# Kernel optimization log

Measured on AMD Instinct MI355X. Metric: run time of the kernel, lower is better.

## Reference

```python
import jax, jax.numpy as jnp
import numpy as np
import math

BS = 8  # JPEG block size
QUALITY = 250.0  # __scale_quality(20) = 5000/20
OFFSET = 128.0 / 255.0


def _dctmtx(bs=BS):
    m = np.empty((bs, bs), dtype=np.float32)
    for j in range(bs):
        for i in range(bs):
            if i == 0:
                m[i, j] = 1.0 / math.sqrt(bs)
            else:
                m[i, j] = math.sqrt(2.0 / bs) * math.cos(math.pi * (2 * j + 1) * i / (2 * bs))
    return jnp.asarray(m)


XFORM = jnp.array([[0.299, 0.587, 0.114],
                   [-0.168735892, -0.331264108, 0.5],
                   [0.5, -0.418687589, -0.081312411]], dtype=jnp.float32)


def setup_inputs() -> dict:
    key = jax.random.key(0)
    k1, k2 = jax.random.split(key)
    rgb = jax.random.uniform(k1, (16, 3, 512, 512), dtype=jnp.float32)
    # qtable: round(abs(t)+0.5)/255 -> positive integers / 255
    quantize = jax.random.randint(k2, (3, BS, BS), 1, 100).astype(jnp.float32) / 255.0
    return {"rgb": rgb, "quantize": quantize}


def _blockify(x, bs=BS):
    # x: [B, H, W] -> [B, H//bs, W//bs, bs, bs]
    b, h, w = x.shape
    return x.reshape(b, h // bs, bs, w // bs, bs).transpose(0, 1, 3, 2, 4)


def reference(rgb, quantize):
    B, C, H, W = rgb.shape
    dct = _dctmtx()
    # RGB -> YCbCr (BHWC matmul with xform^T, expressed on BCHW via einsum)
    ycbcr = jnp.einsum('bchw,kc->bkhw', rgb, XFORM)
    shift = jnp.array([0.0, OFFSET, OFFSET], dtype=rgb.dtype)[None, :, None, None]
    ycbcr = jnp.clip(ycbcr + shift, 0.0, 1.0) - OFFSET
    # chroma 2x2 mean subsample
    y = ycbcr[:, 0]                                            # [B, H, W]
    cbcr = ycbcr[:, 1:].reshape(B, 2, H // 2, 2, W // 2, 2).mean(axis=(3, 5))
    channels = [y, cbcr[:, 0], cbcr[:, 1]]
    outs = []
    for i, ch in enumerate(channels):
        blocks = _blockify(ch)                                 # [B, nh, nw, 8, 8]
        dcts = jnp.einsum('ij,bhwjk,lk->bhwil', dct, blocks, dct)
        denom = quantize[i] * (QUALITY / 100.0) + 0.5 / 255.0  # [8, 8]
        comp = jnp.round(dcts / denom)
        outs.append(comp.reshape(-1, BS, BS))
    return tuple(outs)
```

## Files before the change

kernel.cpp:

```cpp
#include <hip/hip_runtime.h>
#include <math.h>


static __device__ __forceinline__ float clip01(float v) {
    return fminf(fmaxf(v, 0.0f), 1.0f);
}

#define M1f 0.49039264020161522f
#define M2f 0.46193976625564337f
#define M3f 0.41573480615127262f
#define M4f 0.35355339059327376f
#define M5f 0.27778511650980111f
#define M6f 0.19134171618254489f
#define M7f 0.097545161008064134f

static constexpr float Dm[8][8] = {
    { M4f,  M4f,  M4f,  M4f,  M4f,  M4f,  M4f,  M4f},
    { M1f,  M3f,  M5f,  M7f, -M7f, -M5f, -M3f, -M1f},
    { M2f,  M6f, -M6f, -M2f, -M2f, -M6f,  M6f,  M2f},
    { M3f, -M7f, -M1f, -M5f,  M5f,  M1f,  M7f, -M3f},
    { M4f, -M4f, -M4f,  M4f,  M4f, -M4f, -M4f,  M4f},
    { M5f, -M1f,  M7f,  M3f, -M3f, -M7f,  M1f, -M5f},
    { M6f, -M2f,  M2f, -M6f, -M6f,  M2f, -M2f,  M6f},
    { M7f, -M5f,  M3f, -M1f,  M1f, -M3f,  M5f, -M7f},
};

__global__ __launch_bounds__(256)
void jpeg_kernel(const float* __restrict__ rgb, const float* __restrict__ quant,
                 float* __restrict__ out)
{
    __shared__ __align__(16) float smem[3616];
    constexpr int YTT = 0;
    constexpr int CBT = 1152;
    constexpr int CRT = 1472;
    constexpr int QNT = 1792;
    constexpr int TMP = 1984;

    const int t = threadIdx.x;

    if (t < 192) smem[QNT + t] = quant[t];

    const int wg   = blockIdx.x;
    const int b    = wg >> 8;
    const int tile = wg & 255;
    const int th   = tile >> 4;
    const int tw   = tile & 15;

    {
        const int qr = t >> 4;
        const int qc = t & 15;
        const int r0 = 2 * qr, c0 = 2 * qc;
        const float* p = rgb + ((size_t)b * 3) * 262144 + (size_t)(th * 32 + r0) * 512 + (tw * 32 + c0);
        const float2 R0 = *(const float2*)p;
        const float2 R1 = *(const float2*)(p + 512);
        const float2 G0 = *(const float2*)(p + 262144);
        const float2 G1 = *(const float2*)(p + 262144 + 512);
        const float2 B0 = *(const float2*)(p + 524288);
        const float2 B1 = *(const float2*)(p + 524288 + 512);
        const float OFF = (float)(128.0 / 255.0);
        const float rr[4] = {R0.x, R0.y, R1.x, R1.y};
        const float gg[4] = {G0.x, G0.y, G1.x, G1.y};
        const float bb[4] = {B0.x, B0.y, B1.x, B1.y};
        float yv[4], cbv[4], crv[4];
        #pragma unroll
        for (int k = 0; k < 4; ++k) {
            const float r_ = rr[k], g_ = gg[k], b_ = bb[k];
            const float y  = (float)(0.299) * r_ + (float)(0.587) * g_ + (float)(0.114) * b_;
            const float cb = (float)(-0.168735892) * r_ + (float)(-0.331264108) * g_ + 0.5f * b_;
            const float cr = 0.5f * r_ + (float)(-0.418687589) * g_ + (float)(-0.081312411) * b_;
            yv[k]  = clip01(y) - OFF;
            cbv[k] = clip01(cb + OFF);
            crv[k] = clip01(cr + OFF);
        }
        *(float2*)&smem[YTT + c0 * 36 + r0]       = make_float2(yv[0], yv[2]);
        *(float2*)&smem[YTT + (c0 + 1) * 36 + r0] = make_float2(yv[1], yv[3]);
        float sb = cbv[0];
        sb = sb + cbv[1];
        sb = sb + cbv[2];
        sb = sb + cbv[3];
        smem[CBT + qc * 20 + qr] = sb * 0.25f - OFF;
        float sr = crv[0];
        sr = sr + crv[1];
        sr = sr + crv[2];
        sr = sr + crv[3];
        smem[CRT + qc * 20 + qr] = sr * 0.25f - OFF;
    }
    __syncthreads();

    const int w  = t >> 6;
    const int l  = t & 63;
    const int bi = l >> 3;
    const int lc = l & 7;

    if (bi < 6) {
        const int sb = w * 6 + bi;
        int xaddr, ch; size_t obase;
        if (sb < 16) {
            const int sr = sb >> 2, sc = sb & 3;
            xaddr = YTT + (sc * 8 + lc) * 36 + sr * 8; ch = 0;
            obase = (((size_t)(b * 64 + th * 4 + sr)) * 64 + (tw * 4 + sc)) * 64;
        } else if (sb < 20) {
            const int s = sb - 16, sr = s >> 1, sc = s & 1;
            xaddr = CBT + (sc * 8 + lc) * 20 + sr * 8; ch = 1;
            obase = (size_t)4194304 + (((size_t)(b * 32 + th * 2 + sr)) * 32 + (tw * 2 + sc)) * 64;
        } else {
            const int s = sb - 20, sr = s >> 1, sc = s & 1;
            xaddr = CRT + (sc * 8 + lc) * 20 + sr * 8; ch = 2;
            obase = (size_t)5242880 + (((size_t)(b * 32 + th * 2 + sr)) * 32 + (tw * 2 + sc)) * 64;
        }

        float x[8];
        *(float4*)&x[0] = *(const float4*)&smem[xaddr];
        *(float4*)&x[4] = *(const float4*)&smem[xaddr + 4];
        const int tbase = TMP + w * 408 + bi * 68;
        #pragma unroll
        for (int i = 0; i < 8; ++i) {
            float s = 0.0f;
            #pragma unroll
            for (int j = 0; j < 8; ++j) s += Dm[i][j] * x[j];
            smem[tbase + i * 8 + lc] = s;
        }

        float tr[8], q[8];
        *(float4*)&tr[0] = *(const float4*)&smem[tbase + lc * 8];
        *(float4*)&tr[4] = *(const float4*)&smem[tbase + lc * 8 + 4];
        *(float4*)&q[0]  = *(const float4*)&smem[QNT + ch * 64 + lc * 8];
        *(float4*)&q[4]  = *(const float4*)&smem[QNT + ch * 64 + lc * 8 + 4];

        const float qadd = (float)(0.5 / 255.0);
        float o[8];
        #pragma unroll
        for (int cc = 0; cc < 8; ++cc) {
            float s = 0.0f;
            #pragma unroll
            for (int k = 0; k < 8; ++k) s += tr[k] * Dm[cc][k];
            const float den = __fadd_rn(__fmul_rn(q[cc], 2.5f), qadd);
            o[cc] = rintf(s / den);
        }
        float* op = out + obase + lc * 8;
        *(float4*)&op[0] = make_float4(o[0], o[1], o[2], o[3]);
        *(float4*)&op[4] = make_float4(o[4], o[5], o[6], o[7]);
    }
}

extern "C" void kernel_launch(void* const* d_in, const int* in_sizes, int n_in,
                              void* d_out, int out_size, void* d_ws, size_t ws_size,
                              hipStream_t stream) {
    const float* rgb   = (const float*)d_in[0];
    const float* quant = (const float*)d_in[1];
    float* out = (float*)d_out;
    dim3 grid(4096), block(256);
    hipLaunchKernelGGL(jpeg_kernel, grid, block, 0, stream, rgb, quant, out);
}
```

Measured before the change: 17.97 us.

## Split tiles into single-wavefront 16x16 workgroups and drop block barrier

Each 32x32 tile is now handled by four separate 64-thread workgroups, each owning one 16x16 region: four Y blocks plus one Cb and one Cr block. Because the workgroup is a single wavefront, the __syncthreads between the color conversion and the DCT is removed and shared memory shrinks from 3616 to 920 floats. The quantization table is read straight from global memory into registers instead of being staged in LDS, and the global loads are issued earlier so they overlap the address setup. The cost is four times as many workgroups with 25% of lanes idle in the DCT stage, and correctness now depends on implicit wavefront-synchronous ordering of the LDS accesses.

```diff
diff --git a/kernel.cpp b/kernel.cpp
--- a/kernel.cpp
+++ b/kernel.cpp
@@ -25,38 +25,63 @@
     { M7f, -M5f,  M3f, -M1f,  M1f, -M3f,  M5f, -M7f},
 };
 
-__global__ __launch_bounds__(256)
+__global__ __launch_bounds__(64)
 void jpeg_kernel(const float* __restrict__ rgb, const float* __restrict__ quant,
                  float* __restrict__ out)
 {
-    __shared__ __align__(16) float smem[3616];
+    __shared__ __align__(16) float smem[920];
     constexpr int YTT = 0;
-    constexpr int CBT = 1152;
-    constexpr int CRT = 1472;
-    constexpr int QNT = 1792;
-    constexpr int TMP = 1984;
+    constexpr int CBT = 320;
+    constexpr int CRT = 416;
+    constexpr int TMP = 512;
 
-    const int t = threadIdx.x;
+    const int l  = threadIdx.x;
+    const int wg = blockIdx.x;
+    const int w  = wg & 3;
+    const int tw = (wg >> 2) & 15;
+    const int th = (wg >> 6) & 15;
+    const int b  = wg >> 10;
+    const int wr = w >> 1, wc = w & 1;
 
-    if (t < 192) smem[QNT + t] = quant[t];
+    const int qr = l >> 3;
+    const int qc = l & 7;
+    const int bi = l >> 3;
+    const int lc = l & 7;
 
-    const int wg   = blockIdx.x;
-    const int b    = wg >> 8;
-    const int tile = wg & 255;
-    const int th   = tile >> 4;
-    const int tw   = tile & 15;
+    const int prow = th * 32 + wr * 16 + 2 * qr;
+    const int pcol = tw * 32 + wc * 16 + 2 * qc;
+    const float* p = rgb + (size_t)b * 786432 + (size_t)prow * 512 + pcol;
+    const float2 R0 = *(const float2*)p;
+    const float2 R1 = *(const float2*)(p + 512);
+    const float2 G0 = *(const float2*)(p + 262144);
+    const float2 G1 = *(const float2*)(p + 262656);
+    const float2 B0 = *(const float2*)(p + 524288);
+    const float2 B1 = *(const float2*)(p + 524800);
+
+    float q[8];
+    int xaddr = 0; size_t obase = 0;
+    if (bi < 6) {
+        int ch;
+        if (bi < 4) {
+            const int bsr = bi >> 1, bsc = bi & 1;
+            xaddr = YTT + (bsc * 8 + lc) * 20 + bsr * 8; ch = 0;
+            obase = (((size_t)(b * 64 + th * 4 + wr * 2 + bsr)) * 64
+                     + (tw * 4 + wc * 2 + bsc)) * 64;
+        } else if (bi == 4) {
+            xaddr = CBT + lc * 12; ch = 1;
+            obase = (size_t)4194304
+                  + (((size_t)(b * 32 + th * 2 + wr)) * 32 + (tw * 2 + wc)) * 64;
+        } else {
+            xaddr = CRT + lc * 12; ch = 2;
+            obase = (size_t)5242880
+                  + (((size_t)(b * 32 + th * 2 + wr)) * 32 + (tw * 2 + wc)) * 64;
+        }
+        const float* qp = quant + ch * 64 + lc * 8;
+        *(float4*)&q[0] = *(const float4*)qp;
+        *(float4*)&q[4] = *(const float4*)(qp + 4);
+    }
 
     {
-        const int qr = t >> 4;
-        const int qc = t & 15;
-        const int r0 = 2 * qr, c0 = 2 * qc;
-        const float* p = rgb + ((size_t)b * 3) * 262144 + (size_t)(th * 32 + r0) * 512 + (tw * 32 + c0);
-        const float2 R0 = *(const float2*)p;
-        const float2 R1 = *(const float2*)(p + 512);
-        const float2 G0 = *(const float2*)(p + 262144);
-        const float2 G1 = *(const float2*)(p + 262144 + 512);
-        const float2 B0 = *(const float2*)(p + 524288);
-        const float2 B1 = *(const float2*)(p + 524288 + 512);
         const float OFF = (float)(128.0 / 255.0);
         const float rr[4] = {R0.x, R0.y, R1.x, R1.y};
         const float gg[4] = {G0.x, G0.y, G1.x, G1.y};
@@ -72,47 +97,25 @@
             cbv[k] = clip01(cb + OFF);
             crv[k] = clip01(cr + OFF);
         }
-        *(float2*)&smem[YTT + c0 * 36 + r0]       = make_float2(yv[0], yv[2]);
-        *(float2*)&smem[YTT + (c0 + 1) * 36 + r0] = make_float2(yv[1], yv[3]);
+        *(float2*)&smem[YTT + (2 * qc) * 20 + 2 * qr]     = make_float2(yv[0], yv[2]);
+        *(float2*)&smem[YTT + (2 * qc + 1) * 20 + 2 * qr] = make_float2(yv[1], yv[3]);
         float sb = cbv[0];
         sb = sb + cbv[1];
         sb = sb + cbv[2];
         sb = sb + cbv[3];
-        smem[CBT + qc * 20 + qr] = sb * 0.25f - OFF;
+        smem[CBT + qc * 12 + qr] = sb * 0.25f - OFF;
         float sr = crv[0];
         sr = sr + crv[1];
         sr = sr + crv[2];
         sr = sr + crv[3];
-        smem[CRT + qc * 20 + qr] = sr * 0.25f - OFF;
+        smem[CRT + qc * 12 + qr] = sr * 0.25f - OFF;
     }
-    __syncthreads();
-
-    const int w  = t >> 6;
-    const int l  = t & 63;
-    const int bi = l >> 3;
-    const int lc = l & 7;
 
     if (bi < 6) {
-        const int sb = w * 6 + bi;
-        int xaddr, ch; size_t obase;
-        if (sb < 16) {
-            const int sr = sb >> 2, sc = sb & 3;
-            xaddr = YTT + (sc * 8 + lc) * 36 + sr * 8; ch = 0;
-            obase = (((size_t)(b * 64 + th * 4 + sr)) * 64 + (tw * 4 + sc)) * 64;
-        } else if (sb < 20) {
-            const int s = sb - 16, sr = s >> 1, sc = s & 1;
-            xaddr = CBT + (sc * 8 + lc) * 20 + sr * 8; ch = 1;
-            obase = (size_t)4194304 + (((size_t)(b * 32 + th * 2 + sr)) * 32 + (tw * 2 + sc)) * 64;
-        } else {
-            const int s = sb - 20, sr = s >> 1, sc = s & 1;
-            xaddr = CRT + (sc * 8 + lc) * 20 + sr * 8; ch = 2;
-            obase = (size_t)5242880 + (((size_t)(b * 32 + th * 2 + sr)) * 32 + (tw * 2 + sc)) * 64;
-        }
-
         float x[8];
         *(float4*)&x[0] = *(const float4*)&smem[xaddr];
         *(float4*)&x[4] = *(const float4*)&smem[xaddr + 4];
-        const int tbase = TMP + w * 408 + bi * 68;
+        const int tbase = TMP + bi * 68;
         #pragma unroll
         for (int i = 0; i < 8; ++i) {
             float s = 0.0f;
@@ -121,11 +124,9 @@
             smem[tbase + i * 8 + lc] = s;
         }
 
-        float tr[8], q[8];
+        float tr[8];
         *(float4*)&tr[0] = *(const float4*)&smem[tbase + lc * 8];
         *(float4*)&tr[4] = *(const float4*)&smem[tbase + lc * 8 + 4];
-        *(float4*)&q[0]  = *(const float4*)&smem[QNT + ch * 64 + lc * 8];
-        *(float4*)&q[4]  = *(const float4*)&smem[QNT + ch * 64 + lc * 8 + 4];
 
         const float qadd = (float)(0.5 / 255.0);
         float o[8];
@@ -149,6 +150,6 @@
     const float* rgb   = (const float*)d_in[0];
     const float* quant = (const float*)d_in[1];
     float* out = (float*)d_out;
-    dim3 grid(4096), block(256);
+    dim3 grid(16384), block(64);
     hipLaunchKernelGGL(jpeg_kernel, grid, block, 0, stream, rgb, quant, out);
 }
```

Measured after the change: 25.68 us. 42.9% more time.

## Process two tiles per block and prefetch second tile during first DCT

Applied to the files above, without the earlier changes.

Each workgroup now handles two adjacent 32x32 tiles using double-buffered shared memory. The second tile's RGB loads are issued before the first tile's DCT, so global memory latency overlaps with compute. The quantization denominators are computed once and reused for both tiles, and the grid is halved. In exchange, the kernel holds more registers and shared memory per block, which may lower occupancy.

```diff
diff --git a/kernel.cpp b/kernel.cpp
--- a/kernel.cpp
+++ b/kernel.cpp
@@ -25,122 +25,155 @@
     { M7f, -M5f,  M3f, -M1f,  M1f, -M3f,  M5f, -M7f},
 };
 
+struct RGB6 { float2 R0, R1, G0, G1, B0, B1; };
+
+static __device__ __forceinline__ RGB6 load_quad(const float* __restrict__ rgb,
+                                                 int b, int prow, int pcol) {
+    const float* p = rgb + (size_t)b * 786432 + (size_t)prow * 512 + pcol;
+    RGB6 v;
+    v.R0 = *(const float2*)p;
+    v.R1 = *(const float2*)(p + 512);
+    v.G0 = *(const float2*)(p + 262144);
+    v.G1 = *(const float2*)(p + 262656);
+    v.B0 = *(const float2*)(p + 524288);
+    v.B1 = *(const float2*)(p + 524800);
+    return v;
+}
+
+static __device__ __forceinline__ void color_store(const RGB6& v, float* smem,
+    int ybase, int cbbase, int crbase, int qr, int qc)
+{
+    const float OFF = (float)(128.0 / 255.0);
+    const float rr[4] = {v.R0.x, v.R0.y, v.R1.x, v.R1.y};
+    const float gg[4] = {v.G0.x, v.G0.y, v.G1.x, v.G1.y};
+    const float bb[4] = {v.B0.x, v.B0.y, v.B1.x, v.B1.y};
+    float yv[4], cbv[4], crv[4];
+    #pragma unroll
+    for (int k = 0; k < 4; ++k) {
+        const float r_ = rr[k], g_ = gg[k], b_ = bb[k];
+        const float y  = (float)(0.299) * r_ + (float)(0.587) * g_ + (float)(0.114) * b_;
+        const float cb = (float)(-0.168735892) * r_ + (float)(-0.331264108) * g_ + 0.5f * b_;
+        const float cr = 0.5f * r_ + (float)(-0.418687589) * g_ + (float)(-0.081312411) * b_;
+        yv[k]  = clip01(y) - OFF;
+        cbv[k] = clip01(cb + OFF);
+        crv[k] = clip01(cr + OFF);
+    }
+    const int r0 = 2 * qr, c0 = 2 * qc;
+    *(float2*)&smem[ybase + c0 * 36 + r0]       = make_float2(yv[0], yv[2]);
+    *(float2*)&smem[ybase + (c0 + 1) * 36 + r0] = make_float2(yv[1], yv[3]);
+    float sb = cbv[0];
+    sb = sb + cbv[1];
+    sb = sb + cbv[2];
+    sb = sb + cbv[3];
+    smem[cbbase + qc * 20 + qr] = sb * 0.25f - OFF;
+    float sr = crv[0];
+    sr = sr + crv[1];
+    sr = sr + crv[2];
+    sr = sr + crv[3];
+    smem[crbase + qc * 20 + qr] = sr * 0.25f - OFF;
+}
+
+static __device__ __forceinline__ void dct_tile(float* smem, float* __restrict__ out,
+    int ybase, int cbbase, int crbase, int tmpbase, const float* den,
+    int b, int th, int tw, int sb, int lc)
+{
+    int xaddr; size_t obase;
+    if (sb < 16) {
+        const int sr = sb >> 2, sc = sb & 3;
+        xaddr = ybase + (sc * 8 + lc) * 36 + sr * 8;
+        obase = (((size_t)(b * 64 + th * 4 + sr)) * 64 + (tw * 4 + sc)) * 64;
+    } else if (sb < 20) {
+        const int s = sb - 16, sr = s >> 1, sc = s & 1;
+        xaddr = cbbase + (sc * 8 + lc) * 20 + sr * 8;
+        obase = (size_t)4194304 + (((size_t)(b * 32 + th * 2 + sr)) * 32 + (tw * 2 + sc)) * 64;
+    } else {
+        const int s = sb - 20, sr = s >> 1, sc = s & 1;
+        xaddr = crbase + (sc * 8 + lc) * 20 + sr * 8;
+        obase = (size_t)5242880 + (((size_t)(b * 32 + th * 2 + sr)) * 32 + (tw * 2 + sc)) * 64;
+    }
+    float x[8];
+    *(float4*)&x[0] = *(const float4*)&smem[xaddr];
+    *(float4*)&x[4] = *(const float4*)&smem[xaddr + 4];
+    #pragma unroll
+    for (int i = 0; i < 8; ++i) {
+        float s = 0.0f;
+        #pragma unroll
+        for (int j = 0; j < 8; ++j) s += Dm[i][j] * x[j];
+        smem[tmpbase + i * 8 + lc] = s;
+    }
+    float tr[8];
+    *(float4*)&tr[0] = *(const float4*)&smem[tmpbase + lc * 8];
+    *(float4*)&tr[4] = *(const float4*)&smem[tmpbase + lc * 8 + 4];
+    float o[8];
+    #pragma unroll
+    for (int cc = 0; cc < 8; ++cc) {
+        float s = 0.0f;
+        #pragma unroll
+        for (int k = 0; k < 8; ++k) s += tr[k] * Dm[cc][k];
+        o[cc] = rintf(s / den[cc]);
+    }
+    float* op = out + obase + lc * 8;
+    *(float4*)&op[0] = make_float4(o[0], o[1], o[2], o[3]);
+    *(float4*)&op[4] = make_float4(o[4], o[5], o[6], o[7]);
+}
+
 __global__ __launch_bounds__(256)
 void jpeg_kernel(const float* __restrict__ rgb, const float* __restrict__ quant,
                  float* __restrict__ out)
 {
-    __shared__ __align__(16) float smem[3616];
-    constexpr int YTT = 0;
-    constexpr int CBT = 1152;
-    constexpr int CRT = 1472;
-    constexpr int QNT = 1792;
-    constexpr int TMP = 1984;
+    __shared__ __align__(16) float smem[5408];
+    constexpr int YTT0 = 0;
+    constexpr int YTT1 = 1152;
+    constexpr int CBT0 = 2304;
+    constexpr int CBT1 = 2624;
+    constexpr int CRT0 = 2944;
+    constexpr int CRT1 = 3264;
+    constexpr int QNT  = 3584;
+    constexpr int TMP  = 3776;
 
     const int t = threadIdx.x;
 
     if (t < 192) smem[QNT + t] = quant[t];
 
-    const int wg   = blockIdx.x;
-    const int b    = wg >> 8;
-    const int tile = wg & 255;
-    const int th   = tile >> 4;
-    const int tw   = tile & 15;
+    const int pair = blockIdx.x;
+    const int b    = pair >> 7;
+    const int rr_  = (pair << 1) & 255;
+    const int th   = rr_ >> 4;
+    const int twA  = rr_ & 15;
+    const int twB  = twA + 1;
 
-    {
-        const int qr = t >> 4;
-        const int qc = t & 15;
-        const int r0 = 2 * qr, c0 = 2 * qc;
-        const float* p = rgb + ((size_t)b * 3) * 262144 + (size_t)(th * 32 + r0) * 512 + (tw * 32 + c0);
-        const float2 R0 = *(const float2*)p;
-        const float2 R1 = *(const float2*)(p + 512);
-        const float2 G0 = *(const float2*)(p + 262144);
-        const float2 G1 = *(const float2*)(p + 262144 + 512);
-        const float2 B0 = *(const float2*)(p + 524288);
-        const float2 B1 = *(const float2*)(p + 524288 + 512);
-        const float OFF = (float)(128.0 / 255.0);
-        const float rr[4] = {R0.x, R0.y, R1.x, R1.y};
-        const float gg[4] = {G0.x, G0.y, G1.x, G1.y};
-        const float bb[4] = {B0.x, B0.y, B1.x, B1.y};
-        float yv[4], cbv[4], crv[4];
-        #pragma unroll
-        for (int k = 0; k < 4; ++k) {
-            const float r_ = rr[k], g_ = gg[k], b_ = bb[k];
-            const float y  = (float)(0.299) * r_ + (float)(0.587) * g_ + (float)(0.114) * b_;
-            const float cb = (float)(-0.168735892) * r_ + (float)(-0.331264108) * g_ + 0.5f * b_;
-            const float cr = 0.5f * r_ + (float)(-0.418687589) * g_ + (float)(-0.081312411) * b_;
-            yv[k]  = clip01(y) - OFF;
-            cbv[k] = clip01(cb + OFF);
-            crv[k] = clip01(cr + OFF);
-        }
-        *(float2*)&smem[YTT + c0 * 36 + r0]       = make_float2(yv[0], yv[2]);
-        *(float2*)&smem[YTT + (c0 + 1) * 36 + r0] = make_float2(yv[1], yv[3]);
-        float sb = cbv[0];
-        sb = sb + cbv[1];
-        sb = sb + cbv[2];
-        sb = sb + cbv[3];
-        smem[CBT + qc * 20 + qr] = sb * 0.25f - OFF;
-        float sr = crv[0];
-        sr = sr + crv[1];
-        sr = sr + crv[2];
-        sr = sr + crv[3];
-        smem[CRT + qc * 20 + qr] = sr * 0.25f - OFF;
-    }
-    __syncthreads();
-
+    const int qr = t >> 4;
+    const int qc = t & 15;
     const int w  = t >> 6;
     const int l  = t & 63;
     const int bi = l >> 3;
     const int lc = l & 7;
+    const int sb = w * 6 + bi;
+    const int tmpbase = TMP + w * 408 + bi * 68;
 
+    const RGB6 va = load_quad(rgb, b, th * 32 + 2 * qr, twA * 32 + 2 * qc);
+    color_store(va, smem, YTT0, CBT0, CRT0, qr, qc);
+    __syncthreads();
+
+    const RGB6 vb = load_quad(rgb, b, th * 32 + 2 * qr, twB * 32 + 2 * qc);
+
+    float den[8];
     if (bi < 6) {
-        const int sb = w * 6 + bi;
-        int xaddr, ch; size_t obase;
-        if (sb < 16) {
-            const int sr = sb >> 2, sc = sb & 3;
-            xaddr = YTT + (sc * 8 + lc) * 36 + sr * 8; ch = 0;
-            obase = (((size_t)(b * 64 + th * 4 + sr)) * 64 + (tw * 4 + sc)) * 64;
-        } else if (sb < 20) {
-            const int s = sb - 16, sr = s >> 1, sc = s & 1;
-            xaddr = CBT + (sc * 8 + lc) * 20 + sr * 8; ch = 1;
-            obase = (size_t)4194304 + (((size_t)(b * 32 + th * 2 + sr)) * 32 + (tw * 2 + sc)) * 64;
-        } else {
-            const int s = sb - 20, sr = s >> 1, sc = s & 1;
-            xaddr = CRT + (sc * 8 + lc) * 20 + sr * 8; ch = 2;
-            obase = (size_t)5242880 + (((size_t)(b * 32 + th * 2 + sr)) * 32 + (tw * 2 + sc)) * 64;
-        }
+        const int ch = (sb < 16) ? 0 : ((sb < 20) ? 1 : 2);
+        float q[8];
+        *(float4*)&q[0] = *(const float4*)&smem[QNT + ch * 64 + lc * 8];
+        *(float4*)&q[4] = *(const float4*)&smem[QNT + ch * 64 + lc * 8 + 4];
+        const float qadd = (float)(0.5 / 255.0);
+        #pragma unroll
+        for (int cc = 0; cc < 8; ++cc)
+            den[cc] = __fadd_rn(__fmul_rn(q[cc], 2.5f), qadd);
+    }
 
-        float x[8];
-        *(float4*)&x[0] = *(const float4*)&smem[xaddr];
-        *(float4*)&x[4] = *(const float4*)&smem[xaddr + 4];
-        const int tbase = TMP + w * 408 + bi * 68;
-        #pragma unroll
-        for (int i = 0; i < 8; ++i) {
-            float s = 0.0f;
-            #pragma unroll
-            for (int j = 0; j < 8; ++j) s += Dm[i][j] * x[j];
-            smem[tbase + i * 8 + lc] = s;
-        }
+    if (bi < 6) dct_tile(smem, out, YTT0, CBT0, CRT0, tmpbase, den, b, th, twA, sb, lc);
 
-        float tr[8], q[8];
-        *(float4*)&tr[0] = *(const float4*)&smem[tbase + lc * 8];
-        *(float4*)&tr[4] = *(const float4*)&smem[tbase + lc * 8 + 4];
-        *(float4*)&q[0]  = *(const float4*)&smem[QNT + ch * 64 + lc * 8];
-        *(float4*)&q[4]  = *(const float4*)&smem[QNT + ch * 64 + lc * 8 + 4];
-
-        const float qadd = (float)(0.5 / 255.0);
-        float o[8];
-        #pragma unroll
-        for (int cc = 0; cc < 8; ++cc) {
-            float s = 0.0f;
-            #pragma unroll
-            for (int k = 0; k < 8; ++k) s += tr[k] * Dm[cc][k];
-            const float den = __fadd_rn(__fmul_rn(q[cc], 2.5f), qadd);
-            o[cc] = rintf(s / den);
-        }
-        float* op = out + obase + lc * 8;
-        *(float4*)&op[0] = make_float4(o[0], o[1], o[2], o[3]);
-        *(float4*)&op[4] = make_float4(o[4], o[5], o[6], o[7]);
-    }
+    color_store(vb, smem, YTT1, CBT1, CRT1, qr, qc);
+    __syncthreads();
+    if (bi < 6) dct_tile(smem, out, YTT1, CBT1, CRT1, tmpbase, den, b, th, twB, sb, lc);
 }
 
 extern "C" void kernel_launch(void* const* d_in, const int* in_sizes, int n_in,
@@ -149,6 +182,6 @@
     const float* rgb   = (const float*)d_in[0];
     const float* quant = (const float*)d_in[1];
     float* out = (float*)d_out;
-    dim3 grid(4096), block(256);
+    dim3 grid(2048), block(256);
     hipLaunchKernelGGL(jpeg_kernel, grid, block, 0, stream, rgb, quant, out);
 }
```

New measurement: 18.78 us. 1.05x slower.
